# Performance work log

Hardware: AMD Instinct MI355X
Metric: run time of the kernel (lower is better)

Reference implementation:

```python
import jax, jax.numpy as jnp
import numpy as np

B, S, F, H = 4, 2048, 512, 8
EPS = 1e-5

def setup_inputs() -> dict:
    key = jax.random.key(0)
    ks = jax.random.split(key, 7)
    scale = 1.0 / np.sqrt(F)
    x = jax.random.normal(ks[0], (B, S, F), dtype=jnp.float32)
    Wq = jax.random.normal(ks[1], (H, F, F), dtype=jnp.float32) * scale
    Wk = jax.random.normal(ks[2], (H, F, F), dtype=jnp.float32) * scale
    Wv = jax.random.normal(ks[3], (H, F, F), dtype=jnp.float32) * scale
    Wj = jax.random.normal(ks[4], (H * F, F), dtype=jnp.float32) * (1.0 / np.sqrt(H * F))
    gamma = jnp.ones((F,), dtype=jnp.float32)
    beta = jnp.zeros((F,), dtype=jnp.float32)
    return {"x": x, "Wq": Wq, "Wk": Wk, "Wv": Wv, "Wj": Wj, "gamma": gamma, "beta": beta}

def _layernorm(y, gamma, beta):
    mu = jnp.mean(y, axis=-1, keepdims=True)
    var = jnp.mean(jnp.square(y - mu), axis=-1, keepdims=True)  # biased, like torch LN
    return (y - mu) * jax.lax.rsqrt(var + EPS) * gamma + beta

def reference(x, Wq, Wk, Wv, Wj, gamma, beta):
    # per-head full-width projections: [B,H,S,F]
    q = jnp.einsum('bsf,hfe->bhse', x, Wq)
    k = jnp.einsum('bsf,hfe->bhse', x, Wk)
    v = jnp.einsum('bsf,hfe->bhse', x, Wv)
    # NOTE: original has no 1/sqrt(d) scaling
    scores = jnp.einsum('bhse,bhte->bhst', q, k)        # [B,H,S,S]
    attn = jax.nn.softmax(scores, axis=-1)
    z = jnp.einsum('bhst,bhtf->bhsf', attn, v)           # [B,H,S,F]
    z = z + x[:, None, :, :]                             # per-head residual (normalize=False)
    # concat heads along feature dim: head0..headH-1
    zcat = jnp.transpose(z, (0, 2, 1, 3)).reshape(x.shape[0], x.shape[1], -1)  # [B,S,H*F]
    out = zcat @ Wj                                      # joiner, no bias
    # dropout is identity in eval mode
    return _layernorm(x + out, gamma, beta)
```

## Files before the change

### kernel.cpp

```cpp
#include <hip/hip_runtime.h>
#include <hip/hip_bf16.h>

#define BB 4
#define SS 2048
#define FF 512
#define HH 8
#define EPSV 1e-5f

typedef __attribute__((ext_vector_type(8))) short bf16x8;
typedef __attribute__((ext_vector_type(4))) float f32x4;

#define MFMA_B16(a,b,c) __builtin_amdgcn_mfma_f32_16x16x32_bf16((a),(b),(c),0,0,0)

__device__ __forceinline__ short f2bf(float v) {
    union { __hip_bfloat16 b; short s; } u; u.b = __float2bfloat16(v); return u.s;
}
__device__ __forceinline__ float bf2f(short s) {
    union { short s; __hip_bfloat16 b; } u; u.s = s; return __bfloat162float(u.b);
}
__device__ __forceinline__ unsigned pack2(short a, short b) {
    return (unsigned)(unsigned short)a | ((unsigned)(unsigned short)b << 16);
}

__global__ __launch_bounds__(256)
void prep_x_kernel(const float* __restrict__ x, short* __restrict__ xhi, short* __restrict__ xlo)
{
    const int n4 = BB*SS*FF/4;
    for (int i = blockIdx.x*256 + threadIdx.x; i < n4; i += gridDim.x*256) {
        float4 v = *(const float4*)&x[(size_t)i*4];
        short h0=f2bf(v.x),h1=f2bf(v.y),h2=f2bf(v.z),h3=f2bf(v.w);
        uint2 ph, pl;
        ph.x = pack2(h0,h1); ph.y = pack2(h2,h3);
        pl.x = pack2(f2bf(v.x-bf2f(h0)), f2bf(v.y-bf2f(h1)));
        pl.y = pack2(f2bf(v.z-bf2f(h2)), f2bf(v.w-bf2f(h3)));
        *(uint2*)&xhi[(size_t)i*4] = ph;
        *(uint2*)&xlo[(size_t)i*4] = pl;
    }
}

__global__ __launch_bounds__(256)
void prep_t_kernel(const float* __restrict__ in, short* __restrict__ oh, short* __restrict__ ol,
                   int R, int C)
{
    __shared__ float Ts[64][68];
    const int t = threadIdx.x;
    const int c0 = blockIdx.x*64, r0 = blockIdx.y*64;
    const size_t mo = (size_t)blockIdx.z * R * C;
    #pragma unroll
    for (int i = 0; i < 4; ++i) {
        int idx = t + 256*i;
        int rr = idx >> 4, c4 = (idx & 15)*4;
        float4 v = *(const float4*)&in[mo + (size_t)(r0+rr)*C + c0 + c4];
        Ts[rr][c4] = v.x; Ts[rr][c4+1] = v.y; Ts[rr][c4+2] = v.z; Ts[rr][c4+3] = v.w;
    }
    __syncthreads();
    #pragma unroll
    for (int i = 0; i < 4; ++i) {
        int idx = t + 256*i;
        int cc = idx >> 4, k4 = (idx & 15)*4;
        short h[4], l[4];
        #pragma unroll
        for (int j = 0; j < 4; ++j) {
            float v = Ts[k4+j][cc];
            h[j] = f2bf(v); l[j] = f2bf(v - bf2f(h[j]));
        }
        uint2 ph, pl;
        ph.x = pack2(h[0],h[1]); ph.y = pack2(h[2],h[3]);
        pl.x = pack2(l[0],l[1]); pl.y = pack2(l[2],l[3]);
        *(uint2*)&oh[mo + (size_t)(c0+cc)*R + r0 + k4] = ph;
        *(uint2*)&ol[mo + (size_t)(c0+cc)*R + r0 + k4] = pl;
    }
}

__global__ __launch_bounds__(256,1)
void proj_kernel(const short* __restrict__ xhi, const short* __restrict__ xlo,
                 const short* __restrict__ Wth, const short* __restrict__ Wtl,
                 short* __restrict__ Qhi, short* __restrict__ Qlo,
                 short* __restrict__ Khi, short* __restrict__ Klo,
                 short* __restrict__ Vt, int b_base, int nbh)
{
    __shared__ short Ah[128][40], Al[128][40];
    __shared__ short Bh[128][40], Bl[128][40];
    const int t = threadIdx.x, lane = t & 63, w = t >> 6;
    const int l15 = lane & 15, l16 = lane >> 4;
    const int wm = (w >> 1)*64, wn = (w & 1)*64;
    const int n0 = blockIdx.x*128, m0 = blockIdx.y*128;
    const int which = blockIdx.z / nbh;
    const int bh = blockIdx.z % nbh;
    const int h = bh % HH;
    const short* xh = xhi + (size_t)(b_base + bh/HH)*SS*FF;
    const short* xl = xlo + (size_t)(b_base + bh/HH)*SS*FF;
    const short* Bgh = Wth + (size_t)(which*HH + h)*FF*FF;
    const short* Bgl = Wtl + (size_t)(which*HH + h)*FF*FF;

    f32x4 acc[4][4] = {};

    for (int k0 = 0; k0 < FF; k0 += 32) {
        __syncthreads();
        #pragma unroll
        for (int i = 0; i < 2; ++i) {
            int idx = t + 256*i;
            int row = idx >> 2, c8 = (idx & 3)*8;
            *(bf16x8*)&Ah[row][c8] = *(const bf16x8*)&xh[(size_t)(m0+row)*FF + k0 + c8];
            *(bf16x8*)&Al[row][c8] = *(const bf16x8*)&xl[(size_t)(m0+row)*FF + k0 + c8];
            *(bf16x8*)&Bh[row][c8] = *(const bf16x8*)&Bgh[(size_t)(n0+row)*FF + k0 + c8];
            *(bf16x8*)&Bl[row][c8] = *(const bf16x8*)&Bgl[(size_t)(n0+row)*FF + k0 + c8];
        }
        __syncthreads();
        bf16x8 a_h[4], a_l[4], b_h[4], b_l[4];
        #pragma unroll
        for (int mf = 0; mf < 4; ++mf) {
            a_h[mf] = *(const bf16x8*)&Ah[wm + mf*16 + l15][l16*8];
            a_l[mf] = *(const bf16x8*)&Al[wm + mf*16 + l15][l16*8];
        }
        #pragma unroll
        for (int nf = 0; nf < 4; ++nf) {
            b_h[nf] = *(const bf16x8*)&Bh[wn + nf*16 + l15][l16*8];
            b_l[nf] = *(const bf16x8*)&Bl[wn + nf*16 + l15][l16*8];
        }
        #pragma unroll
        for (int mf = 0; mf < 4; ++mf)
        #pragma unroll
        for (int nf = 0; nf < 4; ++nf) {
            acc[mf][nf] = MFMA_B16(a_h[mf], b_h[nf], acc[mf][nf]);
            acc[mf][nf] = MFMA_B16(a_h[mf], b_l[nf], acc[mf][nf]);
            acc[mf][nf] = MFMA_B16(a_l[mf], b_h[nf], acc[mf][nf]);
        }
    }
    if (which < 2) {
        short* Ph = ((which==0) ? Qhi : Khi) + (size_t)bh*SS*FF;
        short* Pl = ((which==0) ? Qlo : Klo) + (size_t)bh*SS*FF;
        #pragma unroll
        for (int mf = 0; mf < 4; ++mf)
        #pragma unroll
        for (int nf = 0; nf < 4; ++nf)
        #pragma unroll
        for (int r = 0; r < 4; ++r) {
            int rw = m0 + wm + mf*16 + l16*4 + r;
            int cl = n0 + wn + nf*16 + l15;
            float v = acc[mf][nf][r];
            short hh = f2bf(v);
            Ph[(size_t)rw*FF + cl] = hh;
            Pl[(size_t)rw*FF + cl] = f2bf(v - bf2f(hh));
        }
    } else {
        short* Vp = Vt + (size_t)bh*FF*SS;
        #pragma unroll
        for (int mf = 0; mf < 4; ++mf)
        #pragma unroll
        for (int nf = 0; nf < 4; ++nf) {
            int cl = n0 + wn + nf*16 + l15;
            int rw = m0 + wm + mf*16 + l16*4;
            uint2 pk;
            pk.x = pack2(f2bf(acc[mf][nf][0]), f2bf(acc[mf][nf][1]));
            pk.y = pack2(f2bf(acc[mf][nf][2]), f2bf(acc[mf][nf][3]));
            *(uint2*)&Vp[(size_t)cl*SS + rw] = pk;
        }
    }
}

__global__ __launch_bounds__(256,1)
void attn_kernel(const float* __restrict__ x,
                 const short* __restrict__ Qhi, const short* __restrict__ Qlo,
                 const short* __restrict__ Khi, const short* __restrict__ Klo,
                 const short* __restrict__ VtG,
                 short* __restrict__ Zhi, short* __restrict__ Zlo, int b_base)
{
    __shared__ short Ksh[32][520], Ksl[32][520];
    __shared__ short Vts[512][40];
    __shared__ float Ps[64][33];
    __shared__ short Pb[64][40];
    __shared__ float mrow[64], lrow[64], srow[64];

    const int t = threadIdx.x, lane = t & 63, w = t >> 6;
    const int l15 = lane & 15, l16 = lane >> 4;
    const int s0 = blockIdx.x * 64;
    const int bh = blockIdx.y;

    const size_t qoff = ((size_t)bh*SS + s0 + w*16 + l15)*FF;
    bf16x8 qh[16], ql[16];
    #pragma unroll
    for (int ks = 0; ks < 16; ++ks) {
        qh[ks] = *(const bf16x8*)&Qhi[qoff + ks*32 + l16*8];
        ql[ks] = *(const bf16x8*)&Qlo[qoff + ks*32 + l16*8];
    }
    if (t < 64) { mrow[t] = -3.0e38f; lrow[t] = 0.0f; }

    const short* Kh = Khi + (size_t)bh*SS*FF;
    const short* Kl = Klo + (size_t)bh*SS*FF;
    const short* Vg = VtG + (size_t)bh*FF*SS;

    f32x4 o[4][8] = {};

    for (int kt = 0; kt < SS/32; ++kt) {
        const int k0 = kt*32;
        #pragma unroll
        for (int i = 0; i < 8; ++i) {
            int idx = t + 256*i;
            int row = idx >> 6, c8 = (idx & 63)*8;
            *(bf16x8*)&Ksh[row][c8] = *(const bf16x8*)&Kh[(size_t)(k0+row)*FF + c8];
            *(bf16x8*)&Ksl[row][c8] = *(const bf16x8*)&Kl[(size_t)(k0+row)*FF + c8];
        }
        __syncthreads();
        f32x4 shh[2] = {}, shl[2] = {}, slh[2] = {};
        #pragma unroll
        for (int ks = 0; ks < 16; ++ks) {
            bf16x8 b0h = *(const bf16x8*)&Ksh[l15][ks*32 + l16*8];
            bf16x8 b0l = *(const bf16x8*)&Ksl[l15][ks*32 + l16*8];
            bf16x8 b1h = *(const bf16x8*)&Ksh[16 + l15][ks*32 + l16*8];
            bf16x8 b1l = *(const bf16x8*)&Ksl[16 + l15][ks*32 + l16*8];
            shh[0] = MFMA_B16(qh[ks], b0h, shh[0]);
            shl[0] = MFMA_B16(qh[ks], b0l, shl[0]);
            slh[0] = MFMA_B16(ql[ks], b0h, slh[0]);
            shh[1] = MFMA_B16(qh[ks], b1h, shh[1]);
            shl[1] = MFMA_B16(qh[ks], b1l, shl[1]);
            slh[1] = MFMA_B16(ql[ks], b1h, slh[1]);
        }
        #pragma unroll
        for (int kf = 0; kf < 2; ++kf) {
            f32x4 sv = shh[kf] + shl[kf] + slh[kf];
            #pragma unroll
            for (int r = 0; r < 4; ++r)
                Ps[w*16 + l16*4 + r][kf*16 + l15] = sv[r];
        }
        bf16x8 vreg[8];
        #pragma unroll
        for (int i = 0; i < 8; ++i) {
            int idx = t + 256*i;
            int f = idx >> 2, c8 = (idx & 3)*8;
            vreg[i] = *(const bf16x8*)&Vg[(size_t)f*SS + k0 + c8];
        }
        __syncthreads();
        #pragma unroll
        for (int i = 0; i < 8; ++i) {
            int idx = t + 256*i;
            int f = idx >> 2, c8 = (idx & 3)*8;
            *(bf16x8*)&Vts[f][c8] = vreg[i];
        }
        {
            const int r = t >> 2, sub = t & 3;
            float sv[8];
            float mx = -3.0e38f;
            #pragma unroll
            for (int j = 0; j < 8; ++j) { sv[j] = Ps[r][sub*8 + j]; mx = fmaxf(mx, sv[j]); }
            mx = fmaxf(mx, __shfl_xor(mx, 1, 4));
            mx = fmaxf(mx, __shfl_xor(mx, 2, 4));
            const float mold = mrow[r];
            const float mnew = fmaxf(mold, mx);
            float ls = 0.0f;
            #pragma unroll
            for (int j = 0; j < 8; ++j) {
                float p = __expf(sv[j] - mnew);
                ls += p;
                Pb[r][sub*8 + j] = f2bf(p);
            }
            ls += __shfl_xor(ls, 1, 4);
            ls += __shfl_xor(ls, 2, 4);
            if (sub == 0) {
                float sc = __expf(mold - mnew);
                srow[r] = sc;
                lrow[r] = lrow[r]*sc + ls;
                mrow[r] = mnew;
            }
        }
        __syncthreads();
        #pragma unroll
        for (int mf = 0; mf < 4; ++mf)
        #pragma unroll
        for (int r = 0; r < 4; ++r) {
            float sc = srow[mf*16 + l16*4 + r];
            #pragma unroll
            for (int ff = 0; ff < 8; ++ff) o[mf][ff][r] *= sc;
        }
        bf16x8 pa[4];
        #pragma unroll
        for (int mf = 0; mf < 4; ++mf)
            pa[mf] = *(const bf16x8*)&Pb[mf*16 + l15][l16*8];
        #pragma unroll
        for (int ff = 0; ff < 8; ++ff) {
            bf16x8 vb = *(const bf16x8*)&Vts[w*128 + ff*16 + l15][l16*8];
            #pragma unroll
            for (int mf = 0; mf < 4; ++mf)
                o[mf][ff] = MFMA_B16(pa[mf], vb, o[mf][ff]);
        }
    }
    const int b = b_base + bh/HH;
    const float* xp = x + ((size_t)b*SS + s0)*FF;
    short* Zh = Zhi + ((size_t)bh*SS + s0)*FF;
    short* Zl = Zlo + ((size_t)bh*SS + s0)*FF;
    #pragma unroll
    for (int mf = 0; mf < 4; ++mf)
    #pragma unroll
    for (int r = 0; r < 4; ++r) {
        const int q = mf*16 + l16*4 + r;
        const float li = 1.0f / lrow[q];
        #pragma unroll
        for (int ff = 0; ff < 8; ++ff) {
            const int col = w*128 + ff*16 + l15;
            float zv = o[mf][ff][r]*li + xp[(size_t)q*FF + col];
            short hh = f2bf(zv);
            Zh[(size_t)q*FF + col] = hh;
            Zl[(size_t)q*FF + col] = f2bf(zv - bf2f(hh));
        }
    }
}

__global__ __launch_bounds__(256,1)
void joiner_kernel(const short* __restrict__ Zhi, const short* __restrict__ Zlo,
                   const short* __restrict__ WjTh, const short* __restrict__ WjTl,
                   float* __restrict__ Jout)
{
    __shared__ short Ah[64][72], Al[64][72];
    __shared__ short Bh[128][72], Bl[128][72];
    const int t = threadIdx.x, lane = t & 63, w = t >> 6;
    const int l15 = lane & 15, l16 = lane >> 4;
    const int wm = (w >> 1)*32, wn = (w & 1)*64;
    const int n0 = blockIdx.x*128, m0 = blockIdx.y*64;
    const int bl = m0 >> 11;
    const int sl = m0 & (SS-1);
    f32x4 acc[2][4] = {};

    for (int k0 = 0; k0 < HH*FF; k0 += 64) {
        const int h = k0 >> 9, f0 = k0 & (FF-1);
        __syncthreads();
        #pragma unroll
        for (int i = 0; i < 2; ++i) {
            int idx = t + 256*i;
            int row = idx >> 3, c8 = (idx & 7)*8;
            size_t g = ((size_t)(bl*HH + h)*SS + sl + row)*FF + f0 + c8;
            *(bf16x8*)&Ah[row][c8] = *(const bf16x8*)&Zhi[g];
            *(bf16x8*)&Al[row][c8] = *(const bf16x8*)&Zlo[g];
        }
        #pragma unroll
        for (int i = 0; i < 4; ++i) {
            int idx = t + 256*i;
            int row = idx >> 3, c8 = (idx & 7)*8;
            size_t g = (size_t)(n0+row)*(HH*FF) + k0 + c8;
            *(bf16x8*)&Bh[row][c8] = *(const bf16x8*)&WjTh[g];
            *(bf16x8*)&Bl[row][c8] = *(const bf16x8*)&WjTl[g];
        }
        __syncthreads();
        #pragma unroll
        for (int ks = 0; ks < 2; ++ks) {
            bf16x8 a_h[2], a_l[2], b_h[4], b_l[4];
            #pragma unroll
            for (int mf = 0; mf < 2; ++mf) {
                a_h[mf] = *(const bf16x8*)&Ah[wm + mf*16 + l15][ks*32 + l16*8];
                a_l[mf] = *(const bf16x8*)&Al[wm + mf*16 + l15][ks*32 + l16*8];
            }
            #pragma unroll
            for (int nf = 0; nf < 4; ++nf) {
                b_h[nf] = *(const bf16x8*)&Bh[wn + nf*16 + l15][ks*32 + l16*8];
                b_l[nf] = *(const bf16x8*)&Bl[wn + nf*16 + l15][ks*32 + l16*8];
            }
            #pragma unroll
            for (int mf = 0; mf < 2; ++mf)
            #pragma unroll
            for (int nf = 0; nf < 4; ++nf) {
                acc[mf][nf] = MFMA_B16(a_h[mf], b_h[nf], acc[mf][nf]);
                acc[mf][nf] = MFMA_B16(a_h[mf], b_l[nf], acc[mf][nf]);
                acc[mf][nf] = MFMA_B16(a_l[mf], b_h[nf], acc[mf][nf]);
            }
        }
    }
    #pragma unroll
    for (int mf = 0; mf < 2; ++mf)
    #pragma unroll
    for (int nf = 0; nf < 4; ++nf)
    #pragma unroll
    for (int r = 0; r < 4; ++r)
        Jout[(size_t)(m0 + wm + mf*16 + l16*4 + r)*FF + n0 + wn + nf*16 + l15] = acc[mf][nf][r];
}

__global__ __launch_bounds__(256)
void ln_kernel(const float* __restrict__ x, const float* __restrict__ Jout,
               const float* __restrict__ gamma, const float* __restrict__ beta,
               float* __restrict__ out, int b_base)
{
    const int t = threadIdx.x, lane = t & 63;
    const int rl = blockIdx.x*4 + (t >> 6);
    const size_t gr = (size_t)b_base*SS + rl;
    const int c1 = lane*4, c2 = 256 + lane*4;
    float4 j1 = *(const float4*)&Jout[(size_t)rl*FF + c1];
    float4 j2 = *(const float4*)&Jout[(size_t)rl*FF + c2];
    float4 x1 = *(const float4*)&x[gr*FF + c1];
    float4 x2 = *(const float4*)&x[gr*FF + c2];
    float y[8];
    y[0]=j1.x+x1.x; y[1]=j1.y+x1.y; y[2]=j1.z+x1.z; y[3]=j1.w+x1.w;
    y[4]=j2.x+x2.x; y[5]=j2.y+x2.y; y[6]=j2.z+x2.z; y[7]=j2.w+x2.w;
    float s1 = 0.f, s2 = 0.f;
    #pragma unroll
    for (int j = 0; j < 8; ++j) { s1 += y[j]; s2 += y[j]*y[j]; }
    #pragma unroll
    for (int m = 1; m < 64; m <<= 1) {
        s1 += __shfl_xor(s1, m);
        s2 += __shfl_xor(s2, m);
    }
    const float mu = s1 * (1.0f/FF);
    float var = s2 * (1.0f/FF) - mu*mu;
    var = fmaxf(var, 0.0f);
    const float rs = rsqrtf(var + EPSV);
    float4 g1 = *(const float4*)&gamma[c1], g2 = *(const float4*)&gamma[c2];
    float4 b1 = *(const float4*)&beta[c1],  b2 = *(const float4*)&beta[c2];
    float4 o1, o2;
    o1.x = (y[0]-mu)*rs*g1.x + b1.x; o1.y = (y[1]-mu)*rs*g1.y + b1.y;
    o1.z = (y[2]-mu)*rs*g1.z + b1.z; o1.w = (y[3]-mu)*rs*g1.w + b1.w;
    o2.x = (y[4]-mu)*rs*g2.x + b2.x; o2.y = (y[5]-mu)*rs*g2.y + b2.y;
    o2.z = (y[6]-mu)*rs*g2.z + b2.z; o2.w = (y[7]-mu)*rs*g2.w + b2.w;
    *(float4*)&out[gr*FF + c1] = o1;
    *(float4*)&out[gr*FF + c2] = o2;
}

extern "C" void kernel_launch(void* const* d_in, const int* in_sizes, int n_in,
                              void* d_out, int out_size, void* d_ws, size_t ws_size,
                              hipStream_t stream)
{
    const float* x     = (const float*)d_in[0];
    const float* Wq    = (const float*)d_in[1];
    const float* Wk    = (const float*)d_in[2];
    const float* Wv    = (const float*)d_in[3];
    const float* Wj    = (const float*)d_in[4];
    const float* gamma = (const float*)d_in[5];
    const float* beta  = (const float*)d_in[6];
    float* out = (float*)d_out;

    short* p = (short*)d_ws;
    short* xhi = p;  p += (size_t)BB*SS*FF;
    short* xlo = p;  p += (size_t)BB*SS*FF;
    short* Wth = p;  p += (size_t)3*HH*FF*FF;
    short* Wtl = p;  p += (size_t)3*HH*FF*FF;
    short* WjTh = p; p += (size_t)HH*FF*FF;
    short* WjTl = p; p += (size_t)HH*FF*FF;
    short* chunk0 = p;

    const size_t head_bytes = (size_t)(chunk0 - (short*)d_ws) * sizeof(short);
    const size_t plane_sh = (size_t)HH*SS*FF;
    const size_t per_batch_bytes = 7*plane_sh*sizeof(short) + (size_t)SS*FF*sizeof(float);
    int nb = 1;
    if (ws_size > head_bytes) {
        size_t m = (ws_size - head_bytes) / per_batch_bytes;
        nb = (m < 1) ? 1 : (m > BB ? BB : (int)m);
    }

    prep_x_kernel<<<2048, 256, 0, stream>>>(x, xhi, xlo);
    prep_t_kernel<<<dim3(8,8,HH), 256, 0, stream>>>(Wq, Wth,                        Wtl,                        FF, FF);
    prep_t_kernel<<<dim3(8,8,HH), 256, 0, stream>>>(Wk, Wth + (size_t)HH*FF*FF,     Wtl + (size_t)HH*FF*FF,     FF, FF);
    prep_t_kernel<<<dim3(8,8,HH), 256, 0, stream>>>(Wv, Wth + (size_t)2*HH*FF*FF,   Wtl + (size_t)2*HH*FF*FF,   FF, FF);
    prep_t_kernel<<<dim3(8,64,1), 256, 0, stream>>>(Wj, WjTh, WjTl, HH*FF, FF);

    for (int b_base = 0; b_base < BB; b_base += nb) {
        int cb = (BB - b_base < nb) ? (BB - b_base) : nb;
        size_t pp = (size_t)cb*plane_sh;
        short* Qhi = chunk0;
        short* Qlo = Qhi + pp;
        short* Khi = Qlo + pp;
        short* Klo = Khi + pp;
        short* Vt  = Klo + pp;
        short* Zhi = Vt  + pp;
        short* Zlo = Zhi + pp;
        float* Jout = (float*)(Zlo + pp);
        const int nbh = cb*HH;

        proj_kernel<<<dim3(4,16,3*nbh), 256, 0, stream>>>(xhi, xlo, Wth, Wtl,
                                                          Qhi, Qlo, Khi, Klo, Vt, b_base, nbh);
        attn_kernel<<<dim3(SS/64, nbh), 256, 0, stream>>>(x, Qhi, Qlo, Khi, Klo, Vt,
                                                          Zhi, Zlo, b_base);
        joiner_kernel<<<dim3(4, cb*SS/64), 256, 0, stream>>>(Zhi, Zlo, WjTh, WjTl, Jout);
        ln_kernel<<<cb*SS/4, 256, 0, stream>>>(x, Jout, gamma, beta, out, b_base);
    }
}
```

Baseline: 1.989 ms.

## Split attention work across 8 waves and raise occupancy hints on GEMM kernels

```diff
diff --git a/kernel.cpp b/kernel.cpp
--- a/kernel.cpp
+++ b/kernel.cpp
@@ -72,7 +72,7 @@
     }
 }
 
-__global__ __launch_bounds__(256,1)
+__global__ __launch_bounds__(256,2)
 void proj_kernel(const short* __restrict__ xhi, const short* __restrict__ xlo,
                  const short* __restrict__ Wth, const short* __restrict__ Wtl,
                  short* __restrict__ Qhi, short* __restrict__ Qlo,
@@ -159,7 +159,7 @@
     }
 }
 
-__global__ __launch_bounds__(256,1)
+__global__ __launch_bounds__(512,2)
 void attn_kernel(const float* __restrict__ x,
                  const short* __restrict__ Qhi, const short* __restrict__ Qlo,
                  const short* __restrict__ Khi, const short* __restrict__ Klo,
@@ -174,10 +174,11 @@
 
     const int t = threadIdx.x, lane = t & 63, w = t >> 6;
     const int l15 = lane & 15, l16 = lane >> 4;
+    const int g = w >> 1, h = w & 1;
     const int s0 = blockIdx.x * 64;
     const int bh = blockIdx.y;
 
-    const size_t qoff = ((size_t)bh*SS + s0 + w*16 + l15)*FF;
+    const size_t qoff = ((size_t)bh*SS + s0 + g*16 + l15)*FF;
     bf16x8 qh[16], ql[16];
     #pragma unroll
     for (int ks = 0; ks < 16; ++ks) {
@@ -190,72 +191,68 @@
     const short* Kl = Klo + (size_t)bh*SS*FF;
     const short* Vg = VtG + (size_t)bh*FF*SS;
 
-    f32x4 o[4][8] = {};
+    f32x4 o[16] = {};
 
     for (int kt = 0; kt < SS/32; ++kt) {
         const int k0 = kt*32;
         #pragma unroll
-        for (int i = 0; i < 8; ++i) {
-            int idx = t + 256*i;
+        for (int i = 0; i < 4; ++i) {
+            int idx = t + 512*i;
             int row = idx >> 6, c8 = (idx & 63)*8;
             *(bf16x8*)&Ksh[row][c8] = *(const bf16x8*)&Kh[(size_t)(k0+row)*FF + c8];
             *(bf16x8*)&Ksl[row][c8] = *(const bf16x8*)&Kl[(size_t)(k0+row)*FF + c8];
         }
         __syncthreads();
-        f32x4 shh[2] = {}, shl[2] = {}, slh[2] = {};
+        f32x4 shh = {}, shl = {}, slh = {};
         #pragma unroll
         for (int ks = 0; ks < 16; ++ks) {
-            bf16x8 b0h = *(const bf16x8*)&Ksh[l15][ks*32 + l16*8];
-            bf16x8 b0l = *(const bf16x8*)&Ksl[l15][ks*32 + l16*8];
-            bf16x8 b1h = *(const bf16x8*)&Ksh[16 + l15][ks*32 + l16*8];
-            bf16x8 b1l = *(const bf16x8*)&Ksl[16 + l15][ks*32 + l16*8];
-            shh[0] = MFMA_B16(qh[ks], b0h, shh[0]);
-            shl[0] = MFMA_B16(qh[ks], b0l, shl[0]);
-            slh[0] = MFMA_B16(ql[ks], b0h, slh[0]);
-            shh[1] = MFMA_B16(qh[ks], b1h, shh[1]);
-            shl[1] = MFMA_B16(qh[ks], b1l, shl[1]);
-            slh[1] = MFMA_B16(ql[ks], b1h, slh[1]);
-        }
-        #pragma unroll
-        for (int kf = 0; kf < 2; ++kf) {
-            f32x4 sv = shh[kf] + shl[kf] + slh[kf];
+            bf16x8 bh8 = *(const bf16x8*)&Ksh[h*16 + l15][ks*32 + l16*8];
+            bf16x8 bl8 = *(const bf16x8*)&Ksl[h*16 + l15][ks*32 + l16*8];
+            shh = MFMA_B16(qh[ks], bh8, shh);
+            shl = MFMA_B16(qh[ks], bl8, shl);
+            slh = MFMA_B16(ql[ks], bh8, slh);
+        }
+        {
+            f32x4 sv = shh + shl + slh;
             #pragma unroll
             for (int r = 0; r < 4; ++r)
-                Ps[w*16 + l16*4 + r][kf*16 + l15] = sv[r];
-        }
-        bf16x8 vreg[8];
-        #pragma unroll
-        for (int i = 0; i < 8; ++i) {
-            int idx = t + 256*i;
+                Ps[g*16 + l16*4 + r][h*16 + l15] = sv[r];
+        }
+        bf16x8 vreg[4];
+        #pragma unroll
+        for (int i = 0; i < 4; ++i) {
+            int idx = t + 512*i;
             int f = idx >> 2, c8 = (idx & 3)*8;
             vreg[i] = *(const bf16x8*)&Vg[(size_t)f*SS + k0 + c8];
         }
         __syncthreads();
         #pragma unroll
-        for (int i = 0; i < 8; ++i) {
-            int idx = t + 256*i;
+        for (int i = 0; i < 4; ++i) {
+            int idx = t + 512*i;
             int f = idx >> 2, c8 = (idx & 3)*8;
             *(bf16x8*)&Vts[f][c8] = vreg[i];
         }
         {
-            const int r = t >> 2, sub = t & 3;
-            float sv[8];
+            const int r = t >> 3, sub = t & 7;
+            float sv[4];
             float mx = -3.0e38f;
             #pragma unroll
-            for (int j = 0; j < 8; ++j) { sv[j] = Ps[r][sub*8 + j]; mx = fmaxf(mx, sv[j]); }
-            mx = fmaxf(mx, __shfl_xor(mx, 1, 4));
-            mx = fmaxf(mx, __shfl_xor(mx, 2, 4));
+            for (int j = 0; j < 4; ++j) { sv[j] = Ps[r][sub*4 + j]; mx = fmaxf(mx, sv[j]); }
+            mx = fmaxf(mx, __shfl_xor(mx, 1, 8));
+            mx = fmaxf(mx, __shfl_xor(mx, 2, 8));
+            mx = fmaxf(mx, __shfl_xor(mx, 4, 8));
             const float mold = mrow[r];
             const float mnew = fmaxf(mold, mx);
             float ls = 0.0f;
             #pragma unroll
-            for (int j = 0; j < 8; ++j) {
+            for (int j = 0; j < 4; ++j) {
                 float p = __expf(sv[j] - mnew);
                 ls += p;
-                Pb[r][sub*8 + j] = f2bf(p);
+                Pb[r][sub*4 + j] = f2bf(p);
             }
-            ls += __shfl_xor(ls, 1, 4);
-            ls += __shfl_xor(ls, 2, 4);
+            ls += __shfl_xor(ls, 1, 8);
+            ls += __shfl_xor(ls, 2, 8);
+            ls += __shfl_xor(ls, 4, 8);
             if (sub == 0) {
                 float sc = __expf(mold - mnew);
                 srow[r] = sc;
@@ -265,23 +262,16 @@
         }
         __syncthreads();
         #pragma unroll
-        for (int mf = 0; mf < 4; ++mf)
-        #pragma unroll
         for (int r = 0; r < 4; ++r) {
-            float sc = srow[mf*16 + l16*4 + r];
-            #pragma unroll
-            for (int ff = 0; ff < 8; ++ff) o[mf][ff][r] *= sc;
-        }
-        bf16x8 pa[4];
-        #pragma unroll
-        for (int mf = 0; mf < 4; ++mf)
-            pa[mf] = *(const bf16x8*)&Pb[mf*16 + l15][l16*8];
-        #pragma unroll
-        for (int ff = 0; ff < 8; ++ff) {
-            bf16x8 vb = *(const bf16x8*)&Vts[w*128 + ff*16 + l15][l16*8];
-            #pragma unroll
-            for (int mf = 0; mf < 4; ++mf)
-                o[mf][ff] = MFMA_B16(pa[mf], vb, o[mf][ff]);
+            float sc = srow[g*16 + l16*4 + r];
+            #pragma unroll
+            for (int ff = 0; ff < 16; ++ff) o[ff][r] *= sc;
+        }
+        bf16x8 pa = *(const bf16x8*)&Pb[g*16 + l15][l16*8];
+        #pragma unroll
+        for (int ff = 0; ff < 16; ++ff) {
+            bf16x8 vb = *(const bf16x8*)&Vts[h*256 + ff*16 + l15][l16*8];
+            o[ff] = MFMA_B16(pa, vb, o[ff]);
         }
     }
     const int b = b_base + bh/HH;
@@ -289,15 +279,13 @@
     short* Zh = Zhi + ((size_t)bh*SS + s0)*FF;
     short* Zl = Zlo + ((size_t)bh*SS + s0)*FF;
     #pragma unroll
-    for (int mf = 0; mf < 4; ++mf)
-    #pragma unroll
     for (int r = 0; r < 4; ++r) {
-        const int q = mf*16 + l16*4 + r;
+        const int q = g*16 + l16*4 + r;
         const float li = 1.0f / lrow[q];
         #pragma unroll
-        for (int ff = 0; ff < 8; ++ff) {
-            const int col = w*128 + ff*16 + l15;
-            float zv = o[mf][ff][r]*li + xp[(size_t)q*FF + col];
+        for (int ff = 0; ff < 16; ++ff) {
+            const int col = h*256 + ff*16 + l15;
+            float zv = o[ff][r]*li + xp[(size_t)q*FF + col];
             short hh = f2bf(zv);
             Zh[(size_t)q*FF + col] = hh;
             Zl[(size_t)q*FF + col] = f2bf(zv - bf2f(hh));
@@ -305,7 +293,7 @@
     }
 }
 
-__global__ __launch_bounds__(256,1)
+__global__ __launch_bounds__(256,2)
 void joiner_kernel(const short* __restrict__ Zhi, const short* __restrict__ Zlo,
                    const short* __restrict__ WjTh, const short* __restrict__ WjTl,
                    float* __restrict__ Jout)
@@ -463,7 +451,7 @@
 
         proj_kernel<<<dim3(4,16,3*nbh), 256, 0, stream>>>(xhi, xlo, Wth, Wtl,
                                                           Qhi, Qlo, Khi, Klo, Vt, b_base, nbh);
-        attn_kernel<<<dim3(SS/64, nbh), 256, 0, stream>>>(x, Qhi, Qlo, Khi, Klo, Vt,
+        attn_kernel<<<dim3(SS/64, nbh), 512, 0, stream>>>(x, Qhi, Qlo, Khi, Klo, Vt,
                                                           Zhi, Zlo, b_base);
         joiner_kernel<<<dim3(4, cb*SS/64), 256, 0, stream>>>(Zhi, Zlo, WjTh, WjTl, Jout);
         ln_kernel<<<cb*SS/4, 256, 0, stream>>>(x, Jout, gamma, beta, out, b_base);
```

After: 2.020 ms. No clear change (+1.5%).
